# Kernel optimization log

Measured on AMD Instinct MI355X. Metric: run time of the kernel, lower is better.

The kernel has to match this reference:

```python
import jax, jax.numpy as jnp
import numpy as np

D = 4  # max horizontal displacement


def setup_inputs() -> dict:
    key = jax.random.key(0)
    k1, k2 = jax.random.split(key)
    feat1 = jax.random.normal(k1, (8, 256, 96, 320), dtype=jnp.float32)
    feat2 = jax.random.normal(k2, (8, 256, 96, 320), dtype=jnp.float32)
    return {"feat1": feat1, "feat2": feat2}


def reference(feat1, feat2):
    B, C, H, W = feat1.shape
    # zero-pad feat2 along width by D on each side
    feat2_padded = jnp.pad(feat2, ((0, 0), (0, 0), (0, 0), (D, D)))
    costs = []
    for i in range(2 * D + 1):  # small fixed loop over 2d+1 shifts
        feat2_slice = jax.lax.dynamic_slice_in_dim(feat2_padded, i, W, axis=3)
        # channel-mean correlation -> (B, H, W)
        costs.append(jnp.mean(feat1 * feat2_slice, axis=1))
    # stack shifts as channels -> (B, 2d+1, H, W)
    return jnp.stack(costs, axis=1)
```

## Files before the change

kernel.cpp:

```cpp
#include <hip/hip_runtime.h>


constexpr int B  = 8;
constexpr int C  = 256;
constexpr int H  = 96;
constexpr int W  = 320;
constexpr int NS = 9;
constexpr int QT = W / 4;
constexpr int RPB = 4;
constexpr int NTH = RPB * QT;
constexpr int NC  = 4;
constexpr int CCH = C / NC;
constexpr int HW  = H * W;
constexpr int OUT_ELEMS = B * NS * H * W;
constexpr int PADW = W + 8;

__global__ void zero_out_kernel(float* __restrict__ out, int n) {
    int i = blockIdx.x * blockDim.x + threadIdx.x;
    int stride = gridDim.x * blockDim.x;
    for (; i < n; i += stride) out[i] = 0.0f;
}

__global__ __launch_bounds__(NTH, 4)
void cv_kernel(const float* __restrict__ f1,
               const float* __restrict__ f2,
               float* __restrict__ part) {
    __shared__ float bufA[RPB][PADW];
    __shared__ float bufB[RPB][PADW];

    const int tid = threadIdx.x;
    const int q   = tid % QT;
    const int r   = tid / QT;

    const int blk    = blockIdx.x;
    const int cchunk = blk % NC;
    const int rowblk = blk / NC;
    const int hb     = rowblk % (H / RPB);
    const int b      = rowblk / (H / RPB);
    const int h      = hb * RPB + r;
    const int c0     = cchunk * CCH;

    const size_t off = ((size_t)(b * C + c0) * H + h) * (size_t)W + 4 * q;
    const float* p1 = f1 + off;
    const float* p2 = f2 + off;

    if (q == 0) {
#pragma unroll
        for (int k = 0; k < 4; ++k) { bufA[r][k] = 0.f; bufB[r][k] = 0.f; }
    }
    if (q == QT - 1) {
#pragma unroll
        for (int k = 0; k < 4; ++k) {
            bufA[r][4 + W + k] = 0.f; bufB[r][4 + W + k] = 0.f;
        }
    }

    float acc[4][NS];
#pragma unroll
    for (int j = 0; j < 4; ++j)
#pragma unroll
        for (int s = 0; s < NS; ++s) acc[j][s] = 0.0f;

    float4 a_cur = *reinterpret_cast<const float4*>(p1);
    float4 r_cur = *reinterpret_cast<const float4*>(p2);
    int cnext = 1;

#define STEP(BUF)                                                          \
    {                                                                      \
        *reinterpret_cast<float4*>(&BUF[r][4 + 4 * q]) = r_cur;            \
        const float4 a_nxt =                                               \
            *reinterpret_cast<const float4*>(p1 + (size_t)cnext * HW);     \
        const float4 r_nxt =                                               \
            *reinterpret_cast<const float4*>(p2 + (size_t)cnext * HW);     \
        cnext = (cnext < CCH - 1) ? cnext + 1 : cnext;                     \
        asm volatile("s_waitcnt lgkmcnt(0)" ::: "memory");                 \
        __builtin_amdgcn_s_barrier();                                      \
        asm volatile("" ::: "memory");                                     \
        const float4 x0 = *reinterpret_cast<const float4*>(&BUF[r][4 * q]);\
        const float4 x2 =                                                  \
            *reinterpret_cast<const float4*>(&BUF[r][4 * q + 8]);          \
        const float xw[12] = {x0.x,  x0.y,  x0.z,  x0.w,                   \
                              r_cur.x, r_cur.y, r_cur.z, r_cur.w,          \
                              x2.x,  x2.y,  x2.z,  x2.w};                  \
        const float av[4] = {a_cur.x, a_cur.y, a_cur.z, a_cur.w};          \
        _Pragma("unroll")                                                  \
        for (int j = 0; j < 4; ++j)                                        \
            _Pragma("unroll")                                              \
            for (int s = 0; s < NS; ++s)                                   \
                acc[j][s] = fmaf(av[j], xw[j + s], acc[j][s]);             \
        a_cur = a_nxt; r_cur = r_nxt;                                      \
    }

#pragma unroll 1
    for (int c = 0; c < CCH; c += 2) {
        STEP(bufA)
        STEP(bufB)
    }
#undef STEP

    float* basep = part + (size_t)cchunk * OUT_ELEMS;
#pragma unroll
    for (int s = 0; s < NS; ++s) {
        float4 v = make_float4(acc[0][s], acc[1][s], acc[2][s], acc[3][s]);
        *reinterpret_cast<float4*>(
            basep + ((size_t)(b * NS + s) * H + h) * (size_t)W + 4 * q) = v;
    }
}

__global__ __launch_bounds__(NTH)
void cv_atomic_kernel(const float* __restrict__ f1,
                      const float* __restrict__ f2,
                      float* __restrict__ out) {
    const int tid = threadIdx.x;
    const int q = tid % QT, r = tid / QT;
    const int blk = blockIdx.x;
    const int cchunk = blk % NC;
    const int rowblk = blk / NC;
    const int hb = rowblk % (H / RPB);
    const int b  = rowblk / (H / RPB);
    const int h  = hb * RPB + r;
    const int c0 = cchunk * CCH;

    const size_t off = ((size_t)(b * C + c0) * H + h) * (size_t)W + 4 * q;
    const float* p1 = f1 + off;
    const float* p2 = f2 + off;
    const bool has_lo = (q > 0), has_hi = (q < QT - 1);
    const int lo = has_lo ? -4 : 0, hi = has_hi ? 4 : 0;

    float acc[4][NS];
#pragma unroll
    for (int j = 0; j < 4; ++j)
#pragma unroll
        for (int s = 0; s < NS; ++s) acc[j][s] = 0.0f;

    for (int c = 0; c < CCH; ++c) {
        float4 a  = *reinterpret_cast<const float4*>(p1);
        float4 x0 = *reinterpret_cast<const float4*>(p2 + lo);
        float4 x1 = *reinterpret_cast<const float4*>(p2);
        float4 x2 = *reinterpret_cast<const float4*>(p2 + hi);
        float x[12] = { has_lo ? x0.x : 0.f, has_lo ? x0.y : 0.f,
                        has_lo ? x0.z : 0.f, has_lo ? x0.w : 0.f,
                        x1.x, x1.y, x1.z, x1.w,
                        has_hi ? x2.x : 0.f, has_hi ? x2.y : 0.f,
                        has_hi ? x2.z : 0.f, has_hi ? x2.w : 0.f };
        float av[4] = {a.x, a.y, a.z, a.w};
#pragma unroll
        for (int j = 0; j < 4; ++j)
#pragma unroll
            for (int s = 0; s < NS; ++s)
                acc[j][s] = fmaf(av[j], x[j + s], acc[j][s]);
        p1 += HW; p2 += HW;
    }
    const float scale = 1.0f / (float)C;
#pragma unroll
    for (int s = 0; s < NS; ++s)
#pragma unroll
        for (int j = 0; j < 4; ++j)
            atomicAdd(out + ((size_t)(b * NS + s) * H + h) * (size_t)W + 4 * q + j,
                      acc[j][s] * scale);
}

__global__ void reduce_kernel(const float* __restrict__ part,
                              float* __restrict__ out, int n4) {
    const float scale = 1.0f / (float)C;
    const float4* p = reinterpret_cast<const float4*>(part);
    float4* o = reinterpret_cast<float4*>(out);
    int i = blockIdx.x * blockDim.x + threadIdx.x;
    int stride = gridDim.x * blockDim.x;
    const int n4e = OUT_ELEMS / 4;
    for (; i < n4; i += stride) {
        float4 v0 = p[i];
        float4 v1 = p[i + n4e];
        float4 v2 = p[i + 2 * n4e];
        float4 v3 = p[i + 3 * n4e];
        float4 rr;
        rr.x = (v0.x + v1.x + v2.x + v3.x) * scale;
        rr.y = (v0.y + v1.y + v2.y + v3.y) * scale;
        rr.z = (v0.z + v1.z + v2.z + v3.z) * scale;
        rr.w = (v0.w + v1.w + v2.w + v3.w) * scale;
        o[i] = rr;
    }
}

extern "C" void kernel_launch(void* const* d_in, const int* in_sizes, int n_in,
                              void* d_out, int out_size, void* d_ws, size_t ws_size,
                              hipStream_t stream) {
    const float* f1 = (const float*)d_in[0];
    const float* f2 = (const float*)d_in[1];
    float* out = (float*)d_out;

    dim3 grid(B * (H / RPB) * NC);
    dim3 block(NTH);

    const size_t need = (size_t)NC * OUT_ELEMS * sizeof(float);
    if (ws_size >= need) {
        float* part = (float*)d_ws;
        hipLaunchKernelGGL(cv_kernel, grid, block, 0, stream, f1, f2, part);
        const int n4 = OUT_ELEMS / 4;
        hipLaunchKernelGGL(reduce_kernel, dim3(2160), dim3(256), 0, stream,
                           part, out, n4);
    } else {
        hipLaunchKernelGGL(zero_out_kernel, dim3(512), dim3(256), 0, stream,
                           out, out_size);
        hipLaunchKernelGGL(cv_atomic_kernel, grid, block, 0, stream, f1, f2, out);
    }
}
```

Measured before the change: 111.8 us.

## Fuse split-channel reduction into main kernel via last-block counter

Replaces the separate reduce kernel with a completion counter per row group: the last of the four channel-chunk blocks to finish sums the partials and writes the scaled output, so the big standalone reduction pass and its launch go away. It also deepens global-load prefetch to three channels ahead, unrolls the channel loop, and remaps block indices so the blocks for one row group spread across XCD-interleaved dispatch. This adds a tiny counter-zeroing launch, threadfence plus atomic overhead, and more registers for the deeper prefetch, which could hurt occupancy.

```diff
diff --git a/kernel.cpp b/kernel.cpp
--- a/kernel.cpp
+++ b/kernel.cpp
@@ -14,6 +14,8 @@
 constexpr int HW  = H * W;
 constexpr int OUT_ELEMS = B * NS * H * W;
 constexpr int PADW = W + 8;
+constexpr int NGRP = B * (H / RPB);
+constexpr int GPX  = NGRP / 8;
 
 __global__ void zero_out_kernel(float* __restrict__ out, int n) {
     int i = blockIdx.x * blockDim.x + threadIdx.x;
@@ -21,24 +23,34 @@
     for (; i < n; i += stride) out[i] = 0.0f;
 }
 
+__global__ void zero_cnt_kernel(int* __restrict__ cnt) {
+    int i = threadIdx.x;
+    if (i < NGRP) cnt[i] = 0;
+}
+
+template <bool FUSED>
 __global__ __launch_bounds__(NTH, 4)
 void cv_kernel(const float* __restrict__ f1,
                const float* __restrict__ f2,
-               float* __restrict__ part) {
+               float* __restrict__ part,
+               int* __restrict__ cnt,
+               float* __restrict__ out) {
     __shared__ float bufA[RPB][PADW];
     __shared__ float bufB[RPB][PADW];
+    __shared__ int last_flag;
 
     const int tid = threadIdx.x;
     const int q   = tid % QT;
     const int r   = tid / QT;
 
-    const int blk    = blockIdx.x;
-    const int cchunk = blk % NC;
-    const int rowblk = blk / NC;
-    const int hb     = rowblk % (H / RPB);
-    const int b      = rowblk / (H / RPB);
-    const int h      = hb * RPB + r;
-    const int c0     = cchunk * CCH;
+    const int x = blockIdx.x & 7;
+    const int m = blockIdx.x >> 3;
+    const int rowblk = x * GPX + (m % GPX);
+    const int cchunk = m / GPX;
+    const int hb = rowblk % (H / RPB);
+    const int b  = rowblk / (H / RPB);
+    const int h  = hb * RPB + r;
+    const int c0 = cchunk * CCH;
 
     const size_t off = ((size_t)(b * C + c0) * H + h) * (size_t)W + 4 * q;
     const float* p1 = f1 + off;
@@ -61,37 +73,44 @@
 #pragma unroll
         for (int s = 0; s < NS; ++s) acc[j][s] = 0.0f;
 
-    float4 a_cur = *reinterpret_cast<const float4*>(p1);
-    float4 r_cur = *reinterpret_cast<const float4*>(p2);
-    int cnext = 1;
+    float4 a0 = *reinterpret_cast<const float4*>(p1);
+    float4 r0 = *reinterpret_cast<const float4*>(p2);
+    float4 a1 = *reinterpret_cast<const float4*>(p1 + (size_t)HW);
+    float4 r1 = *reinterpret_cast<const float4*>(p2 + (size_t)HW);
+    float4 a2 = *reinterpret_cast<const float4*>(p1 + 2 * (size_t)HW);
+    float4 r2 = *reinterpret_cast<const float4*>(p2 + 2 * (size_t)HW);
+
+    const float* pl1 = p1 + 3 * (size_t)HW;
+    const float* pl2 = p2 + 3 * (size_t)HW;
+    int cadv = CCH - 4;
 
 #define STEP(BUF)                                                          \
     {                                                                      \
-        *reinterpret_cast<float4*>(&BUF[r][4 + 4 * q]) = r_cur;            \
-        const float4 a_nxt =                                               \
-            *reinterpret_cast<const float4*>(p1 + (size_t)cnext * HW);     \
-        const float4 r_nxt =                                               \
-            *reinterpret_cast<const float4*>(p2 + (size_t)cnext * HW);     \
-        cnext = (cnext < CCH - 1) ? cnext + 1 : cnext;                     \
+        *reinterpret_cast<float4*>(&BUF[r][4 + 4 * q]) = r0;               \
+        const float4 an = *reinterpret_cast<const float4*>(pl1);           \
+        const float4 rn = *reinterpret_cast<const float4*>(pl2);           \
+        const size_t adv = (cadv > 0) ? (size_t)HW : 0;                    \
+        --cadv;                                                            \
+        pl1 += adv; pl2 += adv;                                            \
         asm volatile("s_waitcnt lgkmcnt(0)" ::: "memory");                 \
         __builtin_amdgcn_s_barrier();                                      \
         asm volatile("" ::: "memory");                                     \
         const float4 x0 = *reinterpret_cast<const float4*>(&BUF[r][4 * q]);\
         const float4 x2 =                                                  \
             *reinterpret_cast<const float4*>(&BUF[r][4 * q + 8]);          \
-        const float xw[12] = {x0.x,  x0.y,  x0.z,  x0.w,                   \
-                              r_cur.x, r_cur.y, r_cur.z, r_cur.w,          \
-                              x2.x,  x2.y,  x2.z,  x2.w};                  \
-        const float av[4] = {a_cur.x, a_cur.y, a_cur.z, a_cur.w};          \
+        const float xw[12] = {x0.x, x0.y, x0.z, x0.w,                      \
+                              r0.x, r0.y, r0.z, r0.w,                      \
+                              x2.x, x2.y, x2.z, x2.w};                     \
+        const float av[4] = {a0.x, a0.y, a0.z, a0.w};                      \
         _Pragma("unroll")                                                  \
         for (int j = 0; j < 4; ++j)                                        \
             _Pragma("unroll")                                              \
             for (int s = 0; s < NS; ++s)                                   \
                 acc[j][s] = fmaf(av[j], xw[j + s], acc[j][s]);             \
-        a_cur = a_nxt; r_cur = r_nxt;                                      \
-    }
-
-#pragma unroll 1
+        a0 = a1; r0 = r1; a1 = a2; r1 = r2; a2 = an; r2 = rn;              \
+    }
+
+#pragma unroll 3
     for (int c = 0; c < CCH; c += 2) {
         STEP(bufA)
         STEP(bufB)
@@ -105,59 +124,33 @@
         *reinterpret_cast<float4*>(
             basep + ((size_t)(b * NS + s) * H + h) * (size_t)W + 4 * q) = v;
     }
-}
-
-__global__ __launch_bounds__(NTH)
-void cv_atomic_kernel(const float* __restrict__ f1,
-                      const float* __restrict__ f2,
-                      float* __restrict__ out) {
-    const int tid = threadIdx.x;
-    const int q = tid % QT, r = tid / QT;
-    const int blk = blockIdx.x;
-    const int cchunk = blk % NC;
-    const int rowblk = blk / NC;
-    const int hb = rowblk % (H / RPB);
-    const int b  = rowblk / (H / RPB);
-    const int h  = hb * RPB + r;
-    const int c0 = cchunk * CCH;
-
-    const size_t off = ((size_t)(b * C + c0) * H + h) * (size_t)W + 4 * q;
-    const float* p1 = f1 + off;
-    const float* p2 = f2 + off;
-    const bool has_lo = (q > 0), has_hi = (q < QT - 1);
-    const int lo = has_lo ? -4 : 0, hi = has_hi ? 4 : 0;
-
-    float acc[4][NS];
-#pragma unroll
-    for (int j = 0; j < 4; ++j)
-#pragma unroll
-        for (int s = 0; s < NS; ++s) acc[j][s] = 0.0f;
-
-    for (int c = 0; c < CCH; ++c) {
-        float4 a  = *reinterpret_cast<const float4*>(p1);
-        float4 x0 = *reinterpret_cast<const float4*>(p2 + lo);
-        float4 x1 = *reinterpret_cast<const float4*>(p2);
-        float4 x2 = *reinterpret_cast<const float4*>(p2 + hi);
-        float x[12] = { has_lo ? x0.x : 0.f, has_lo ? x0.y : 0.f,
-                        has_lo ? x0.z : 0.f, has_lo ? x0.w : 0.f,
-                        x1.x, x1.y, x1.z, x1.w,
-                        has_hi ? x2.x : 0.f, has_hi ? x2.y : 0.f,
-                        has_hi ? x2.z : 0.f, has_hi ? x2.w : 0.f };
-        float av[4] = {a.x, a.y, a.z, a.w};
-#pragma unroll
-        for (int j = 0; j < 4; ++j)
-#pragma unroll
-            for (int s = 0; s < NS; ++s)
-                acc[j][s] = fmaf(av[j], x[j + s], acc[j][s]);
-        p1 += HW; p2 += HW;
-    }
-    const float scale = 1.0f / (float)C;
-#pragma unroll
-    for (int s = 0; s < NS; ++s)
-#pragma unroll
-        for (int j = 0; j < 4; ++j)
-            atomicAdd(out + ((size_t)(b * NS + s) * H + h) * (size_t)W + 4 * q + j,
-                      acc[j][s] * scale);
+
+    if (FUSED) {
+        __threadfence();
+        if (tid == 0) {
+            int old = atomicAdd(&cnt[rowblk], 1);
+            last_flag = (old == NC - 1) ? 1 : 0;
+        }
+        __syncthreads();
+        if (last_flag) {
+            __threadfence();
+            const float scale = 1.0f / (float)C;
+#pragma unroll
+            for (int s = 0; s < NS; ++s) {
+                const size_t o = ((size_t)(b * NS + s) * H + h) * (size_t)W + 4 * q;
+                float4 v0 = *reinterpret_cast<const float4*>(part + o);
+                float4 v1 = *reinterpret_cast<const float4*>(part + (size_t)OUT_ELEMS + o);
+                float4 v2 = *reinterpret_cast<const float4*>(part + 2 * (size_t)OUT_ELEMS + o);
+                float4 v3 = *reinterpret_cast<const float4*>(part + 3 * (size_t)OUT_ELEMS + o);
+                float4 rr;
+                rr.x = (v0.x + v1.x + v2.x + v3.x) * scale;
+                rr.y = (v0.y + v1.y + v2.y + v3.y) * scale;
+                rr.z = (v0.z + v1.z + v2.z + v3.z) * scale;
+                rr.w = (v0.w + v1.w + v2.w + v3.w) * scale;
+                *reinterpret_cast<float4*>(out + o) = rr;
+            }
+        }
+    }
 }
 
 __global__ void reduce_kernel(const float* __restrict__ part,
@@ -182,6 +175,59 @@
     }
 }
 
+__global__ __launch_bounds__(NTH)
+void cv_atomic_kernel(const float* __restrict__ f1,
+                      const float* __restrict__ f2,
+                      float* __restrict__ out) {
+    const int tid = threadIdx.x;
+    const int q = tid % QT, r = tid / QT;
+    const int blk = blockIdx.x;
+    const int cchunk = blk % NC;
+    const int rowblk = blk / NC;
+    const int hb = rowblk % (H / RPB);
+    const int b  = rowblk / (H / RPB);
+    const int h  = hb * RPB + r;
+    const int c0 = cchunk * CCH;
+
+    const size_t off = ((size_t)(b * C + c0) * H + h) * (size_t)W + 4 * q;
+    const float* p1 = f1 + off;
+    const float* p2 = f2 + off;
+    const bool has_lo = (q > 0), has_hi = (q < QT - 1);
+    const int lo = has_lo ? -4 : 0, hi = has_hi ? 4 : 0;
+
+    float acc[4][NS];
+#pragma unroll
+    for (int j = 0; j < 4; ++j)
+#pragma unroll
+        for (int s = 0; s < NS; ++s) acc[j][s] = 0.0f;
+
+    for (int c = 0; c < CCH; ++c) {
+        float4 a  = *reinterpret_cast<const float4*>(p1);
+        float4 x0 = *reinterpret_cast<const float4*>(p2 + lo);
+        float4 x1 = *reinterpret_cast<const float4*>(p2);
+        float4 x2 = *reinterpret_cast<const float4*>(p2 + hi);
+        float xw[12] = { has_lo ? x0.x : 0.f, has_lo ? x0.y : 0.f,
+                         has_lo ? x0.z : 0.f, has_lo ? x0.w : 0.f,
+                         x1.x, x1.y, x1.z, x1.w,
+                         has_hi ? x2.x : 0.f, has_hi ? x2.y : 0.f,
+                         has_hi ? x2.z : 0.f, has_hi ? x2.w : 0.f };
+        float av[4] = {a.x, a.y, a.z, a.w};
+#pragma unroll
+        for (int j = 0; j < 4; ++j)
+#pragma unroll
+            for (int s = 0; s < NS; ++s)
+                acc[j][s] = fmaf(av[j], xw[j + s], acc[j][s]);
+        p1 += HW; p2 += HW;
+    }
+    const float scale = 1.0f / (float)C;
+#pragma unroll
+    for (int s = 0; s < NS; ++s)
+#pragma unroll
+        for (int j = 0; j < 4; ++j)
+            atomicAdd(out + ((size_t)(b * NS + s) * H + h) * (size_t)W + 4 * q + j,
+                      acc[j][s] * scale);
+}
+
 extern "C" void kernel_launch(void* const* d_in, const int* in_sizes, int n_in,
                               void* d_out, int out_size, void* d_ws, size_t ws_size,
                               hipStream_t stream) {
@@ -192,13 +238,21 @@
     dim3 grid(B * (H / RPB) * NC);
     dim3 block(NTH);
 
-    const size_t need = (size_t)NC * OUT_ELEMS * sizeof(float);
-    if (ws_size >= need) {
+    const size_t need_part = (size_t)NC * OUT_ELEMS * sizeof(float);
+    const size_t need_full = need_part + NGRP * sizeof(int) + 256;
+
+    if (ws_size >= need_full) {
         float* part = (float*)d_ws;
-        hipLaunchKernelGGL(cv_kernel, grid, block, 0, stream, f1, f2, part);
-        const int n4 = OUT_ELEMS / 4;
+        int* cnt = (int*)((char*)d_ws + need_part);
+        hipLaunchKernelGGL(zero_cnt_kernel, dim3(1), dim3(256), 0, stream, cnt);
+        hipLaunchKernelGGL((cv_kernel<true>), grid, block, 0, stream,
+                           f1, f2, part, cnt, out);
+    } else if (ws_size >= need_part) {
+        float* part = (float*)d_ws;
+        hipLaunchKernelGGL((cv_kernel<false>), grid, block, 0, stream,
+                           f1, f2, part, nullptr, out);
         hipLaunchKernelGGL(reduce_kernel, dim3(2160), dim3(256), 0, stream,
-                           part, out, n4);
+                           part, out, OUT_ELEMS / 4);
     } else {
         hipLaunchKernelGGL(zero_out_kernel, dim3(512), dim3(256), 0, stream,
                            out, out_size);
```

New measurement: 380.4 us, median of 5. 240% more time.
